# Kernel tuning notes

Measured on AMD Instinct MI355X. Metric: run time of the kernel, lower is better.

The kernel has to match this reference:

```python
import jax, jax.numpy as jnp
import numpy as np

EPS = 1e-5
N_HEADS = 8
CLAMP = 100.0


def layernorm(x, g, b):
    m = x.mean(-1, keepdims=True)
    v = x.var(-1, keepdims=True)  # biased var, matches torch LayerNorm
    return (x - m) / jnp.sqrt(v + EPS) * g + b


def depthwise7(x, w, b):
    # x: [B,C,H,W], w: [C,1,7,7] depthwise (groups=C), pad=3
    y = jax.lax.conv_general_dilated(
        x, w, window_strides=(1, 1), padding=[(3, 3), (3, 3)],
        dimension_numbers=('NCHW', 'OIHW', 'NCHW'),
        feature_group_count=x.shape[1])
    return y + b[None, :, None, None]


def setup_inputs() -> dict:
    key = jax.random.key(0)
    ks = jax.random.split(key, 12)
    B, N, C = 8, 4096, 512
    KH = 7
    s = 0.02
    return {
        'x': jax.random.normal(ks[0], (B, N, C), jnp.float32),
        'qkv_w': jax.random.normal(ks[1], (C, 3 * C), jnp.float32) * s,
        'qkv_b': jnp.zeros((3 * C,), jnp.float32),
        'out_w': jax.random.normal(ks[2], (C, C), jnp.float32) * s,
        'out_b': jnp.zeros((C,), jnp.float32),
        'pre_g': jnp.ones((C,), jnp.float32),
        'pre_b': jnp.zeros((C,), jnp.float32),
        'lcm_g': jnp.ones((C,), jnp.float32),
        'lcm_b': jnp.zeros((C,), jnp.float32),
        'ci_w': jax.random.normal(ks[3], (C, 1, KH, KH), jnp.float32) * s,
        'ci_b': jnp.zeros((C,), jnp.float32),
        'bn_g': jnp.ones((C,), jnp.float32),
        'bn_b': jnp.zeros((C,), jnp.float32),
        'co_w': jax.random.normal(ks[4], (C, 1, KH, KH), jnp.float32) * s,
        'co_b': jnp.zeros((C,), jnp.float32),
        'H': 64,
        'W': 64,
    }


def reference(x, qkv_w, qkv_b, out_w, out_b, pre_g, pre_b, lcm_g, lcm_b,
              ci_w, ci_b, bn_g, bn_b, co_w, co_b, H, W):
    B, N, C = x.shape
    hd = C // N_HEADS
    normed = layernorm(x, pre_g, pre_b)
    qkv = normed @ qkv_w + qkv_b                       # [B,N,3C]
    qkv = qkv.reshape(B, N, 3, N_HEADS, hd).transpose(2, 0, 3, 1, 4)
    q = jax.nn.relu(qkv[0])                            # [B,h,N,d]
    k = jax.nn.relu(qkv[1])
    v = qkv[2]
    kv = jnp.einsum('bhnd,bhnv->bhdv', k, v)           # O(N d^2) associativity trick
    normalizer = jnp.maximum(k.sum(2, keepdims=True), CLAMP)  # [B,h,1,d]
    attn = jnp.einsum('bhnd,bhdv->bhnv', q, kv)
    denom = jnp.maximum((q * normalizer).sum(-1, keepdims=True), CLAMP)
    attn = attn / denom
    attn = attn.transpose(0, 2, 1, 3).reshape(B, N, C)
    attn = attn @ out_w + out_b
    # Local Concentration Module on lcm_norm(attn)
    t = layernorm(attn, lcm_g, lcm_b)
    xi = t.transpose(0, 2, 1).reshape(B, C, H, W)
    y = depthwise7(xi, ci_w, ci_b)
    y = jax.nn.gelu(y, approximate=False)
    m = y.mean((0, 2, 3), keepdims=True)               # BatchNorm2d training-mode stats
    var = y.var((0, 2, 3), keepdims=True)
    y = (y - m) / jnp.sqrt(var + EPS) * bn_g[None, :, None, None] + bn_b[None, :, None, None]
    y = depthwise7(y, co_w, co_b)
    lcm_out = y.reshape(B, C, N).transpose(0, 2, 1)
    return x + attn + lcm_out
```

## Files before the change

kernel.cpp:

```cpp
#include <hip/hip_runtime.h>
#include <math.h>

typedef short v8s __attribute__((ext_vector_type(8)));
typedef short v4s __attribute__((ext_vector_type(4)));
typedef float v4f __attribute__((ext_vector_type(4)));

__device__ __forceinline__ float b2f(unsigned short u) {
    return __uint_as_float(((unsigned)u) << 16);
}
__device__ __forceinline__ unsigned short f2b(float f) {
    unsigned u = __float_as_uint(f);
    unsigned r = (u + 0x7FFF + ((u >> 16) & 1)) >> 16;
    return (unsigned short)r;
}
__device__ __forceinline__ int swz8(int row) { return (row & 7) ^ ((row >> 3) & 7); }

__device__ __forceinline__ void gl_lds16(const unsigned short* g, unsigned short* l) {
    __builtin_amdgcn_global_load_lds(
        (const __attribute__((address_space(1))) void*)g,
        (__attribute__((address_space(3))) void*)l,
        16, 0, 0);
}

__global__ __launch_bounds__(256) void zero_fill(float* __restrict__ p, int n) {
    int i = blockIdx.x * 256 + threadIdx.x;
    if (i < n) p[i] = 0.0f;
}

__global__ __launch_bounds__(256) void ln_apply(const float* __restrict__ x,
                                                const float* __restrict__ g,
                                                const float* __restrict__ bt,
                                                unsigned short* __restrict__ out) {
    size_t row = blockIdx.x;
    const float2* p = (const float2*)(x + row * 512);
    int t = threadIdx.x;
    float2 v = p[t];
    float s = v.x + v.y, s2 = v.x * v.x + v.y * v.y;
    for (int o = 32; o > 0; o >>= 1) {
        s += __shfl_down(s, o);
        s2 += __shfl_down(s2, o);
    }
    __shared__ float rs[4], rq[4];
    int wave = t >> 6, lane = t & 63;
    if (lane == 0) { rs[wave] = s; rq[wave] = s2; }
    __syncthreads();
    float ts = rs[0] + rs[1] + rs[2] + rs[3];
    float tq = rq[0] + rq[1] + rq[2] + rq[3];
    float mean = ts * (1.0f / 512.0f);
    float var = tq * (1.0f / 512.0f) - mean * mean;
    float inv = rsqrtf(var + 1e-5f);
    float2 gg = ((const float2*)g)[t];
    float2 bb = ((const float2*)bt)[t];
    ushort2 o2;
    o2.x = f2b((v.x - mean) * inv * gg.x + bb.x);
    o2.y = f2b((v.y - mean) * inv * gg.y + bb.y);
    *(ushort2*)&out[row * 512 + 2 * t] = o2;
}

__global__ __launch_bounds__(256) void transpose_f2b(const float* __restrict__ in,
                                                     unsigned short* __restrict__ out,
                                                     int R, int C) {
    __shared__ unsigned short tile[32][33];
    int c0 = blockIdx.x * 32, r0 = blockIdx.y * 32;
    int tx = threadIdx.x, ty = threadIdx.y;
    for (int j = 0; j < 32; j += 8)
        tile[ty + j][tx] = f2b(in[(size_t)(r0 + ty + j) * C + c0 + tx]);
    __syncthreads();
    for (int j = 0; j < 32; j += 8)
        out[(size_t)(c0 + ty + j) * R + r0 + tx] = tile[tx][ty + j];
}

template <int NB, bool QKV>
__global__ __launch_bounds__(512, 4) void gemm256(const unsigned short* __restrict__ A,
                                                  const unsigned short* __restrict__ Bt,
                                                  const float* __restrict__ bias,
                                                  unsigned short* __restrict__ o0,
                                                  unsigned short* __restrict__ o1,
                                                  unsigned short* __restrict__ o2) {
    __shared__ __align__(16) unsigned short LB[3][12288];
    int t = threadIdx.x;
    int wave = t >> 6, lane = t & 63;
    int wm = wave >> 1, wn = wave & 1;
    int mrow = lane & 15, kq4 = lane >> 4;
    int nwg = gridDim.x;
    int cpx = nwg >> 3;
    int bid = blockIdx.x;
    int swz = (bid & 7) * cpx + (bid >> 3);
    int n0 = (swz % NB) * 128;
    int m0 = (swz / NB) * 256;
    const unsigned short* Ab = A + (size_t)m0 * 512;
    const unsigned short* Bb = Bt + (size_t)n0 * 512;
    int rA0 = t >> 2;
    int cA0 = (((t & 3) ^ ((rA0 >> 1) & 3)) * 8);
    int rA1 = 128 + (t >> 2);
    int cA1 = (((t & 3) ^ ((rA1 >> 1) & 3)) * 8);
    size_t srcA0 = (size_t)rA0 * 512 + cA0;
    size_t srcA1 = (size_t)rA1 * 512 + cA1;
    unsigned offA0 = wave * 512;
    unsigned offA1 = 4096 + wave * 512;
    unsigned offB  = 8192 + wave * 512;
    v4f acc[4][4] = {};
    int swr = ((kq4 ^ ((mrow >> 1) & 3)) * 8);

#define STAGE(kt, slot)                                          \
    do {                                                         \
        const unsigned short* aS = Ab + (size_t)(kt) * 32;       \
        const unsigned short* bS = Bb + (size_t)(kt) * 32;       \
        gl_lds16(aS + srcA0, &LB[slot][offA0]);                  \
        gl_lds16(aS + srcA1, &LB[slot][offA1]);                  \
        gl_lds16(bS + srcA0, &LB[slot][offB]);                   \
    } while (0)

    STAGE(0, 0);
    STAGE(1, 1);
    for (int kt = 0; kt < 16; ++kt) {
        if (kt < 15) {
            asm volatile("s_waitcnt vmcnt(3)" ::: "memory");
        } else {
            asm volatile("s_waitcnt vmcnt(0)" ::: "memory");
        }
        __builtin_amdgcn_s_barrier();
        asm volatile("" ::: "memory");
        if (kt + 2 < 16) STAGE(kt + 2, (kt + 2) % 3);
        const unsigned short* as = LB[kt % 3];
        const unsigned short* bs = LB[kt % 3] + 8192;
        v8s af[4], bf[4];
#pragma unroll
        for (int i = 0; i < 4; i++)
            af[i] = *(const v8s*)&as[(wm * 64 + i * 16 + mrow) * 32 + swr];
#pragma unroll
        for (int j = 0; j < 4; j++)
            bf[j] = *(const v8s*)&bs[(wn * 64 + j * 16 + mrow) * 32 + swr];
        __builtin_amdgcn_s_setprio(1);
#pragma unroll
        for (int i = 0; i < 4; i++)
#pragma unroll
            for (int j = 0; j < 4; j++)
                acc[i][j] = __builtin_amdgcn_mfma_f32_16x16x32_bf16(af[i], bf[j], acc[i][j], 0, 0, 0);
        __builtin_amdgcn_s_setprio(0);
    }
#undef STAGE
    __syncthreads();
    unsigned short* CT = &LB[0][0];
    bool doRelu = QKV && (n0 < 1024);
#pragma unroll
    for (int j = 0; j < 4; j++) {
        int col = wn * 64 + j * 16 + mrow;
        float bv = bias[n0 + col];
        int gr = col >> 3, gb = col & 7;
#pragma unroll
        for (int i = 0; i < 4; i++) {
            int rowb = wm * 64 + i * 16 + kq4 * 4;
#pragma unroll
            for (int r = 0; r < 4; r++) {
                int row = rowb + r;
                float v = acc[i][j][r] + bv;
                if (doRelu) v = fmaxf(v, 0.0f);
                CT[row * 136 + ((gr ^ swz8(row)) << 3) + gb] = f2b(v);
            }
        }
    }
    __syncthreads();
    if (!QKV || n0 < 512) {
#pragma unroll
        for (int p = 0; p < 8; p++) {
            int g = p * 512 + t;
            int row = g >> 4, gl = g & 15;
            v8s v = *(const v8s*)&CT[row * 136 + ((gl ^ swz8(row)) << 3)];
            *(v8s*)&o0[(size_t)(m0 + row) * 512 + n0 + gl * 8] = v;
        }
    } else {
        unsigned short* Tb = (n0 < 1024) ? o1 : o2;
        int col = t >> 2, sub = t & 3;
        int cglob = n0 + col;
        int hl = (cglob & 511) >> 6, d = cglob & 63;
        int bb = m0 >> 12, gc = m0 & 4095;
        unsigned short* dst = Tb + ((size_t)((bb * 8 + hl) * 64 + d)) * 4096 + gc;
        int cg = col >> 3, cb7 = col & 7;
#pragma unroll
        for (int g = 0; g < 8; g++) {
            v8s v;
#pragma unroll
            for (int e = 0; e < 8; e++) {
                int rr = g * 32 + sub * 8 + e;
                v[e] = (short)CT[rr * 136 + ((cg ^ swz8(rr)) << 3) + cb7];
            }
            *(v8s*)&dst[g * 32 + sub * 8] = v;
        }
    }
}

__global__ __launch_bounds__(256) void kv_part(const unsigned short* __restrict__ kT,
                                               const unsigned short* __restrict__ vT,
                                               float* __restrict__ kvp,
                                               float* __restrict__ ksp) {
    __shared__ __align__(16) unsigned short LB[3][4096];
    int bh = blockIdx.x, nc = blockIdx.y;
    int t = threadIdx.x;
    int w = t >> 6, lane = t & 63;
    int wdk = w >> 1, wdv = w & 1;
    int mrow = lane & 15, kq4 = lane >> 4;
    const unsigned short* Kb = kT + (size_t)bh * 262144 + nc * 512;
    const unsigned short* Vb = vT + (size_t)bh * 262144 + nc * 512;
    int rA = t >> 2;
    int lcA = (t & 3) ^ (rA & 3);
    size_t srcoff = (size_t)rA * 4096 + lcA * 8;
    unsigned dstK = w * 512;
    unsigned dstV = 2048 + w * 512;
    v4f acc[2][2] = {};
    v4f accs[2] = {};
    v8s ones;
#pragma unroll
    for (int jj = 0; jj < 8; jj++) ones[jj] = (short)0x3F80;

#define KSTAGE(ks, slot)                                         \
    do {                                                         \
        gl_lds16(Kb + (size_t)(ks) * 32 + srcoff, &LB[slot][dstK]); \
        gl_lds16(Vb + (size_t)(ks) * 32 + srcoff, &LB[slot][dstV]); \
    } while (0)

    KSTAGE(0, 0);
    KSTAGE(1, 1);
    for (int ks = 0; ks < 16; ++ks) {
        if (ks < 15) {
            asm volatile("s_waitcnt vmcnt(2)" ::: "memory");
        } else {
            asm volatile("s_waitcnt vmcnt(0)" ::: "memory");
        }
        __builtin_amdgcn_s_barrier();
        asm volatile("" ::: "memory");
        if (ks + 2 < 16) KSTAGE(ks + 2, (ks + 2) % 3);
        const unsigned short* as = LB[ks % 3];
        v8s af[2], bf[2];
#pragma unroll
        for (int i = 0; i < 2; i++) {
            int row = wdk * 32 + i * 16 + mrow;
            af[i] = *(const v8s*)&as[row * 32 + ((kq4 ^ (row & 3)) << 3)];
        }
#pragma unroll
        for (int j = 0; j < 2; j++) {
            int row = wdv * 32 + j * 16 + mrow;
            bf[j] = *(const v8s*)&as[2048 + row * 32 + ((kq4 ^ (row & 3)) << 3)];
        }
#pragma unroll
        for (int i = 0; i < 2; i++)
#pragma unroll
            for (int j = 0; j < 2; j++)
                acc[i][j] = __builtin_amdgcn_mfma_f32_16x16x32_bf16(af[i], bf[j], acc[i][j], 0, 0, 0);
        if (wdv == 0) {
#pragma unroll
            for (int i = 0; i < 2; i++)
                accs[i] = __builtin_amdgcn_mfma_f32_16x16x32_bf16(af[i], ones, accs[i], 0, 0, 0);
        }
    }
#undef KSTAGE
    float* dst = kvp + ((size_t)(bh * 8 + nc)) * 4096;
#pragma unroll
    for (int i = 0; i < 2; i++)
#pragma unroll
        for (int j = 0; j < 2; j++)
#pragma unroll
            for (int r = 0; r < 4; r++) {
                int row = wdk * 32 + i * 16 + kq4 * 4 + r;
                int col = wdv * 32 + j * 16 + mrow;
                dst[row * 64 + col] = acc[i][j][r];
            }
    if (wdv == 0 && mrow == 0) {
        float* kd = ksp + ((size_t)(bh * 8 + nc)) * 64 + wdk * 32;
#pragma unroll
        for (int i = 0; i < 2; i++)
#pragma unroll
            for (int r = 0; r < 4; r++)
                kd[i * 16 + kq4 * 4 + r] = accs[i][r];
    }
}

__global__ __launch_bounds__(256) void kv_reduce(const float* __restrict__ kvp,
                                                 const float* __restrict__ ksp,
                                                 float* __restrict__ kvb,
                                                 float* __restrict__ ksum) {
    int tid = blockIdx.x * 256 + threadIdx.x;
    int bh = tid >> 12, e = tid & 4095;
    float s = 0.0f;
#pragma unroll
    for (int c = 0; c < 8; c++) s += kvp[((size_t)(bh * 8 + c)) * 4096 + e];
    kvb[(size_t)bh * 4096 + e] = s;
    if (tid < 4096) {
        int bh2 = tid >> 6, dk = tid & 63;
        float x = 0.0f;
#pragma unroll
        for (int c = 0; c < 8; c++) x += ksp[(bh2 * 8 + c) * 64 + dk];
        ksum[tid] = x;
    }
}

__global__ __launch_bounds__(256) void attn_mfma(unsigned short* __restrict__ qa,
                                                 const float* __restrict__ kv,
                                                 const float* __restrict__ ksum) {
    __shared__ __align__(16) unsigned short olds[4][4096];
    int bh = blockIdx.y;
    int b = bh >> 3, h = bh & 7;
    int t = threadIdx.x;
    int w = t >> 6, lane = t & 63;
    int mrow = lane & 15, kq4 = lane >> 6 ? 0 : lane >> 4;
    kq4 = lane >> 4;
    int nb = blockIdx.x * 256 + w * 64;
    unsigned short* qbase = qa + ((size_t)(b * 4096 + nb)) * 512 + h * 64;
    const float* kvb = kv + (size_t)bh * 4096;
    v4f acc[4][4] = {};
    v4f accd[4] = {};
#pragma unroll
    for (int s = 0; s < 2; s++) {
        v8s af[4];
#pragma unroll
        for (int i = 0; i < 4; i++)
            af[i] = *(const v8s*)&qbase[(size_t)(i * 16 + mrow) * 512 + s * 32 + kq4 * 8];
        v8s nh, nl;
#pragma unroll
        for (int jj = 0; jj < 8; jj++) {
            float nv = fmaxf(ksum[bh * 64 + s * 32 + kq4 * 8 + jj], 100.0f);
            unsigned short hb = f2b(nv);
            nh[jj] = (short)hb;
            nl[jj] = (short)f2b(nv - b2f(hb));
        }
#pragma unroll
        for (int i = 0; i < 4; i++) {
            accd[i] = __builtin_amdgcn_mfma_f32_16x16x32_bf16(af[i], nh, accd[i], 0, 0, 0);
            accd[i] = __builtin_amdgcn_mfma_f32_16x16x32_bf16(af[i], nl, accd[i], 0, 0, 0);
        }
#pragma unroll
        for (int j = 0; j < 4; j++) {
            v8s kh, kl;
#pragma unroll
            for (int jj = 0; jj < 8; jj++) {
                float kvv = kvb[(size_t)(s * 32 + kq4 * 8 + jj) * 64 + j * 16 + mrow];
                unsigned short hb = f2b(kvv);
                kh[jj] = (short)hb;
                kl[jj] = (short)f2b(kvv - b2f(hb));
            }
#pragma unroll
            for (int i = 0; i < 4; i++) {
                acc[i][j] = __builtin_amdgcn_mfma_f32_16x16x32_bf16(af[i], kh, acc[i][j], 0, 0, 0);
                acc[i][j] = __builtin_amdgcn_mfma_f32_16x16x32_bf16(af[i], kl, acc[i][j], 0, 0, 0);
            }
        }
    }
    unsigned short* ol = olds[w];
#pragma unroll
    for (int i = 0; i < 4; i++) {
        float inv[4];
#pragma unroll
        for (int r = 0; r < 4; r++) inv[r] = 1.0f / fmaxf(accd[i][r], 100.0f);
#pragma unroll
        for (int j = 0; j < 4; j++) {
            int dv = j * 16 + mrow;
#pragma unroll
            for (int r = 0; r < 4; r++) {
                int rl = i * 16 + kq4 * 4 + r;
                ol[rl * 64 + (((dv >> 3) ^ (rl & 7)) << 3) + (dv & 7)] = f2b(acc[i][j][r] * inv[r]);
            }
        }
    }
    __syncthreads();
#pragma unroll
    for (int p = 0; p < 8; p++) {
        int idx = p * 64 + lane;
        int row = idx >> 3, gl = idx & 7;
        v8s v = *(const v8s*)&ol[row * 64 + ((gl ^ (row & 7)) << 3)];
        *(v8s*)&qbase[(size_t)row * 512 + gl * 8] = v;
    }
}

__global__ __launch_bounds__(256) void ln2_transpose(const unsigned short* __restrict__ in,
                                                     const float* __restrict__ g,
                                                     const float* __restrict__ bt,
                                                     unsigned short* __restrict__ out) {
    int bid = blockIdx.x;
    int b = bid >> 6;
    int n0 = (bid & 63) * 64;
    __shared__ float gs[512], bs[512];
    __shared__ __align__(16) unsigned short tile[512 * 64];
    int t = threadIdx.x;
    for (int i = t; i < 512; i += 256) { gs[i] = g[i]; bs[i] = bt[i]; }
    int nl = t >> 2, sub = t & 3;
    const unsigned short* src = in + ((size_t)(b * 4096 + n0 + nl)) * 512 + sub * 8;
    v8s vv[16];
#pragma unroll
    for (int c16 = 0; c16 < 16; c16++)
        vv[c16] = *(const v8s*)&src[c16 * 32];
    float s = 0.f, s2 = 0.f;
#pragma unroll
    for (int c16 = 0; c16 < 16; c16++)
#pragma unroll
        for (int j = 0; j < 8; j++) {
            float f = b2f((unsigned short)vv[c16][j]);
            s += f; s2 += f * f;
        }
    s += __shfl_xor(s, 1); s2 += __shfl_xor(s2, 1);
    s += __shfl_xor(s, 2); s2 += __shfl_xor(s2, 2);
    float mean = s * (1.f / 512.f);
    float var = s2 * (1.f / 512.f) - mean * mean;
    float inv = rsqrtf(var + 1e-5f);
    __syncthreads();
#pragma unroll
    for (int c16 = 0; c16 < 16; c16++) {
        int cb_ = sub * 8 + c16 * 32;
#pragma unroll
        for (int j = 0; j < 8; j++) {
            int c = cb_ + j;
            float f = b2f((unsigned short)vv[c16][j]);
            float y = (f - mean) * inv * gs[c] + bs[c];
            tile[c * 64 + ((((nl >> 3) ^ (c & 7)) << 3) | (nl & 7))] = f2b(y);
        }
    }
    __syncthreads();
    unsigned short* dst = out + ((size_t)b * 512) * 4096 + n0;
#pragma unroll
    for (int p = 0; p < 16; p++) {
        int chunk = p * 256 + t;
        int c = chunk >> 3, gseg = chunk & 7;
        int phys = gseg ^ (c & 7);
        v8s v = *(const v8s*)&tile[c * 64 + phys * 8];
        *(v8s*)&dst[(size_t)c * 4096 + gseg * 8] = v;
    }
}

__global__ __launch_bounds__(256) void dwconv7_gelu(const unsigned short* __restrict__ in,
                                                    const float* __restrict__ w,
                                                    const float* __restrict__ bias,
                                                    unsigned short* __restrict__ out,
                                                    float* __restrict__ bn_sum,
                                                    float* __restrict__ bn_sumsq) {
    int bc = blockIdx.x;
    int c = bc & 511;
    __shared__ float img[70 * 72];
    __shared__ float wsm[49];
    __shared__ float r1[4], r2[4];
    int t = threadIdx.x;
    int tx = t & 63, ty = t >> 6;
    for (int i = t; i < 70 * 72; i += 256) img[i] = 0.0f;
    if (t < 49) wsm[t] = w[c * 49 + t];
    __syncthreads();
    const unsigned short* src = in + (size_t)bc * 4096;
#pragma unroll
    for (int q = t; q < 512; q += 256) {
        v8s v = *(const v8s*)&src[q * 8];
        float* ip = &img[((q >> 3) + 3) * 72 + (q & 7) * 8 + 3];
#pragma unroll
        for (int j = 0; j < 8; j++) ip[j] = b2f((unsigned short)v[j]);
    }
    __syncthreads();
    float wt[49];
#pragma unroll
    for (int i = 0; i < 49; i++) wt[i] = wsm[i];
    float bv = bias[c];
    float acc[16];
#pragma unroll
    for (int i = 0; i < 16; i++) acc[i] = bv;
    int h0 = ty * 16;
#pragma unroll
    for (int rr = 0; rr < 22; rr++) {
        float v[7];
#pragma unroll
        for (int kw = 0; kw < 7; kw++) v[kw] = img[(h0 + rr) * 72 + tx + kw];
#pragma unroll
        for (int kh = 0; kh < 7; kh++) {
            int o = rr - kh;
            if (o >= 0 && o <= 15) {
                float dot = v[0] * wt[kh * 7];
#pragma unroll
                for (int kw = 1; kw < 7; kw++) dot += v[kw] * wt[kh * 7 + kw];
                acc[o] += dot;
            }
        }
    }
    float s = 0.0f, s2 = 0.0f;
    unsigned short* dst = out + (size_t)bc * 4096;
#pragma unroll
    for (int i = 0; i < 16; i++) {
        float a = acc[i];
        float ge = 0.5f * a * (1.0f + erff(a * 0.70710678118f));
        dst[(h0 + i) * 64 + tx] = f2b(ge);
        s += ge;
        s2 += ge * ge;
    }
    for (int o = 32; o > 0; o >>= 1) {
        s += __shfl_down(s, o);
        s2 += __shfl_down(s2, o);
    }
    int lane = t & 63;
    if (lane == 0) { r1[ty] = s; r2[ty] = s2; }
    __syncthreads();
    if (t == 0) {
        atomicAdd(&bn_sum[c], r1[0] + r1[1] + r1[2] + r1[3]);
        atomicAdd(&bn_sumsq[c], r2[0] + r2[1] + r2[2] + r2[3]);
    }
}

__global__ void bn_finalize(const float* __restrict__ s, const float* __restrict__ s2,
                            const float* __restrict__ g, const float* __restrict__ b,
                            float2* __restrict__ ab) {
    int c = blockIdx.x * blockDim.x + threadIdx.x;
    if (c >= 512) return;
    float m = s[c] * (1.0f / 32768.0f);
    float var = s2[c] * (1.0f / 32768.0f) - m * m;
    float inv = rsqrtf(var + 1e-5f);
    float sc = g[c] * inv;
    ab[c] = make_float2(sc, b[c] - m * sc);
}

__global__ __launch_bounds__(256) void dwconv7_bn(const unsigned short* __restrict__ in,
                                                  const float2* __restrict__ bnab,
                                                  const float* __restrict__ w,
                                                  const float* __restrict__ bias,
                                                  unsigned short* __restrict__ out) {
    int bc = blockIdx.x;
    int c = bc & 511;
    __shared__ float img[70 * 72];
    __shared__ float wsm[49];
    int t = threadIdx.x;
    int tx = t & 63, ty = t >> 6;
    for (int i = t; i < 70 * 72; i += 256) img[i] = 0.0f;
    if (t < 49) wsm[t] = w[c * 49 + t];
    __syncthreads();
    float2 ab = bnab[c];
    const unsigned short* src = in + (size_t)bc * 4096;
#pragma unroll
    for (int q = t; q < 512; q += 256) {
        v8s v = *(const v8s*)&src[q * 8];
        float* ip = &img[((q >> 3) + 3) * 72 + (q & 7) * 8 + 3];
#pragma unroll
        for (int j = 0; j < 8; j++) ip[j] = b2f((unsigned short)v[j]) * ab.x + ab.y;
    }
    __syncthreads();
    float wt[49];
#pragma unroll
    for (int i = 0; i < 49; i++) wt[i] = wsm[i];
    float bv = bias[c];
    float acc[16];
#pragma unroll
    for (int i = 0; i < 16; i++) acc[i] = bv;
    int h0 = ty * 16;
#pragma unroll
    for (int rr = 0; rr < 22; rr++) {
        float v[7];
#pragma unroll
        for (int kw = 0; kw < 7; kw++) v[kw] = img[(h0 + rr) * 72 + tx + kw];
#pragma unroll
        for (int kh = 0; kh < 7; kh++) {
            int o = rr - kh;
            if (o >= 0 && o <= 15) {
                float dot = v[0] * wt[kh * 7];
#pragma unroll
                for (int kw = 1; kw < 7; kw++) dot += v[kw] * wt[kh * 7 + kw];
                acc[o] += dot;
            }
        }
    }
    unsigned short* dst = out + (size_t)bc * 4096;
#pragma unroll
    for (int i = 0; i < 16; i++)
        dst[(h0 + i) * 64 + tx] = f2b(acc[i]);
}

__global__ __launch_bounds__(256) void final_add(const float* __restrict__ x,
                                                 const unsigned short* __restrict__ attn,
                                                 const unsigned short* __restrict__ y2,
                                                 float* __restrict__ out) {
    __shared__ unsigned short tile[32][36];
    int b = blockIdx.z;
    int c0 = blockIdx.x * 32, n0 = blockIdx.y * 32;
    int t = threadIdx.x;
    {
        int c = t >> 3, n4 = (t & 7) * 4;
        ushort4 v = *(const ushort4*)&y2[((size_t)(b * 512 + c0 + c)) * 4096 + n0 + n4];
        tile[c][n4] = v.x; tile[c][n4 + 1] = v.y; tile[c][n4 + 2] = v.z; tile[c][n4 + 3] = v.w;
    }
    __syncthreads();
    int nl = t >> 3, cl = (t & 7) * 4;
    size_t idx = ((size_t)(b * 4096 + n0 + nl)) * 512 + c0 + cl;
    float4 xv = *(const float4*)&x[idx];
    ushort4 av = *(const ushort4*)&attn[idx];
    float4 o;
    o.x = xv.x + b2f(av.x) + b2f(tile[cl][nl]);
    o.y = xv.y + b2f(av.y) + b2f(tile[cl + 1][nl]);
    o.z = xv.z + b2f(av.z) + b2f(tile[cl + 2][nl]);
    o.w = xv.w + b2f(av.w) + b2f(tile[cl + 3][nl]);
    *(float4*)&out[idx] = o;
}

extern "C" void kernel_launch(void* const* d_in, const int* in_sizes, int n_in,
                              void* d_out, int out_size, void* d_ws, size_t ws_size,
                              hipStream_t stream) {
    const float* x     = (const float*)d_in[0];
    const float* qkv_w = (const float*)d_in[1];
    const float* qkv_b = (const float*)d_in[2];
    const float* out_w = (const float*)d_in[3];
    const float* out_b = (const float*)d_in[4];
    const float* pre_g = (const float*)d_in[5];
    const float* pre_b = (const float*)d_in[6];
    const float* lcm_g = (const float*)d_in[7];
    const float* lcm_b = (const float*)d_in[8];
    const float* ci_w  = (const float*)d_in[9];
    const float* ci_b  = (const float*)d_in[10];
    const float* bn_g  = (const float*)d_in[11];
    const float* bn_b  = (const float*)d_in[12];
    const float* co_w  = (const float*)d_in[13];
    const float* co_b  = (const float*)d_in[14];

    char* ws = (char*)d_ws;
    const size_t SLOT = 33554432;
    unsigned short* S0 = (unsigned short*)(ws);
    unsigned short* S1 = (unsigned short*)(ws + SLOT);
    unsigned short* S2 = (unsigned short*)(ws + 2 * SLOT);
    const size_t MISC = 3 * SLOT;
    unsigned short* wT1 = (unsigned short*)(ws + MISC);
    unsigned short* wT2 = (unsigned short*)(ws + MISC + 1572864);
    float* kvb          = (float*)(ws + MISC + 2097152);
    float* ksum         = (float*)(ws + MISC + 2097152 + 1048576);
    float* bn_sum       = (float*)(ws + MISC + 2097152 + 1048576 + 16384);
    float* bn_sumsq     = (float*)(ws + MISC + 2097152 + 1048576 + 16384 + 2048);
    float2* bnab        = (float2*)(ws + MISC + 3166208);
    float* ksp          = (float*)(ws + MISC + 3170304);
    float* outp         = (float*)d_out;

    unsigned short* normed = (unsigned short*)d_out;
    float* kvp             = (float*)((char*)d_out + SLOT);

    dim3 tb(32, 8);
    transpose_f2b<<<dim3(48, 16), tb, 0, stream>>>(qkv_w, wT1, 512, 1536);
    transpose_f2b<<<dim3(16, 16), tb, 0, stream>>>(out_w, wT2, 512, 512);
    zero_fill<<<4, 256, 0, stream>>>(bn_sum, 1024);
    ln_apply<<<32768, 256, 0, stream>>>(x, pre_g, pre_b, normed);
    gemm256<12, true><<<1536, 512, 0, stream>>>(normed, wT1, qkv_b, S0, S1, S2);
    kv_part<<<dim3(64, 8), 256, 0, stream>>>(S1, S2, kvp, ksp);
    kv_reduce<<<1024, 256, 0, stream>>>(kvp, ksp, kvb, ksum);
    attn_mfma<<<dim3(16, 64), 256, 0, stream>>>(S0, kvb, ksum);
    gemm256<4, false><<<512, 512, 0, stream>>>(S0, wT2, out_b, S1, S1, S1);
    ln2_transpose<<<512, 256, 0, stream>>>(S1, lcm_g, lcm_b, S0);
    dwconv7_gelu<<<4096, 256, 0, stream>>>(S0, ci_w, ci_b, S2, bn_sum, bn_sumsq);
    bn_finalize<<<2, 256, 0, stream>>>(bn_sum, bn_sumsq, bn_g, bn_b, bnab);
    dwconv7_bn<<<4096, 256, 0, stream>>>(S2, bnab, co_w, co_b, S0);
    final_add<<<dim3(16, 128, 8), tb.x * tb.y, 0, stream>>>(x, S1, S0, outp);
}
```

Before: 436.5 us.

## Double-buffer GEMM fragments, one-wave LayerNorm rows, precomputed split-bf16 kv, bigger final_add blocks

The GEMM main loop now preloads the next k-step's LDS fragments into registers between two halves of the MFMAs. This hides LDS read latency behind matrix math, at the cost of more registers. LayerNorm now processes one row per wave with 8 elements per lane, dropping the shared-memory reduction and block barrier. kv_reduce now writes the kv matrix and the clamped normalizer pre-split into high and low bf16 halves in transposed layout, so attn_mfma does vector loads instead of per-element strided loads and conversions. final_add handles four tiles per block to cut the launch block count.

```diff
diff --git a/kernel.cpp b/kernel.cpp
--- a/kernel.cpp
+++ b/kernel.cpp
@@ -31,30 +31,36 @@
                                                 const float* __restrict__ g,
                                                 const float* __restrict__ bt,
                                                 unsigned short* __restrict__ out) {
-    size_t row = blockIdx.x;
-    const float2* p = (const float2*)(x + row * 512);
-    int t = threadIdx.x;
-    float2 v = p[t];
-    float s = v.x + v.y, s2 = v.x * v.x + v.y * v.y;
+    int t = threadIdx.x;
+    int lane = t & 63, wave = t >> 6;
+    size_t row = (size_t)blockIdx.x * 4 + wave;
+    const float* p = x + row * 512 + lane * 8;
+    float4 va = *(const float4*)p;
+    float4 vb = *(const float4*)(p + 4);
+    float s = va.x + va.y + va.z + va.w + vb.x + vb.y + vb.z + vb.w;
+    float s2 = va.x * va.x + va.y * va.y + va.z * va.z + va.w * va.w +
+               vb.x * vb.x + vb.y * vb.y + vb.z * vb.z + vb.w * vb.w;
     for (int o = 32; o > 0; o >>= 1) {
-        s += __shfl_down(s, o);
-        s2 += __shfl_down(s2, o);
-    }
-    __shared__ float rs[4], rq[4];
-    int wave = t >> 6, lane = t & 63;
-    if (lane == 0) { rs[wave] = s; rq[wave] = s2; }
-    __syncthreads();
-    float ts = rs[0] + rs[1] + rs[2] + rs[3];
-    float tq = rq[0] + rq[1] + rq[2] + rq[3];
-    float mean = ts * (1.0f / 512.0f);
-    float var = tq * (1.0f / 512.0f) - mean * mean;
+        s += __shfl_xor(s, o);
+        s2 += __shfl_xor(s2, o);
+    }
+    float mean = s * (1.0f / 512.0f);
+    float var = s2 * (1.0f / 512.0f) - mean * mean;
     float inv = rsqrtf(var + 1e-5f);
-    float2 gg = ((const float2*)g)[t];
-    float2 bb = ((const float2*)bt)[t];
-    ushort2 o2;
-    o2.x = f2b((v.x - mean) * inv * gg.x + bb.x);
-    o2.y = f2b((v.y - mean) * inv * gg.y + bb.y);
-    *(ushort2*)&out[row * 512 + 2 * t] = o2;
+    float4 g0 = *(const float4*)(g + lane * 8);
+    float4 g1 = *(const float4*)(g + lane * 8 + 4);
+    float4 b0 = *(const float4*)(bt + lane * 8);
+    float4 b1 = *(const float4*)(bt + lane * 8 + 4);
+    v8s o8;
+    o8[0] = (short)f2b((va.x - mean) * inv * g0.x + b0.x);
+    o8[1] = (short)f2b((va.y - mean) * inv * g0.y + b0.y);
+    o8[2] = (short)f2b((va.z - mean) * inv * g0.z + b0.z);
+    o8[3] = (short)f2b((va.w - mean) * inv * g0.w + b0.w);
+    o8[4] = (short)f2b((vb.x - mean) * inv * g1.x + b1.x);
+    o8[5] = (short)f2b((vb.y - mean) * inv * g1.y + b1.y);
+    o8[6] = (short)f2b((vb.z - mean) * inv * g1.z + b1.z);
+    o8[7] = (short)f2b((vb.w - mean) * inv * g1.w + b1.w);
+    *(v8s*)&out[row * 512 + lane * 8] = o8;
 }
 
 __global__ __launch_bounds__(256) void transpose_f2b(const float* __restrict__ in,
@@ -113,31 +119,57 @@
 
     STAGE(0, 0);
     STAGE(1, 1);
+    asm volatile("s_waitcnt vmcnt(3)" ::: "memory");
+    __builtin_amdgcn_s_barrier();
+    asm volatile("" ::: "memory");
+    v8s cA[4], cB[4];
+    {
+        const unsigned short* as = LB[0];
+        const unsigned short* bs = as + 8192;
+#pragma unroll
+        for (int i = 0; i < 4; i++) {
+            cA[i] = *(const v8s*)&as[(wm * 64 + i * 16 + mrow) * 32 + swr];
+            cB[i] = *(const v8s*)&bs[(wn * 64 + i * 16 + mrow) * 32 + swr];
+        }
+    }
+#pragma unroll
     for (int kt = 0; kt < 16; ++kt) {
-        if (kt < 15) {
-            asm volatile("s_waitcnt vmcnt(3)" ::: "memory");
-        } else {
-            asm volatile("s_waitcnt vmcnt(0)" ::: "memory");
-        }
         __builtin_amdgcn_s_barrier();
         asm volatile("" ::: "memory");
         if (kt + 2 < 16) STAGE(kt + 2, (kt + 2) % 3);
-        const unsigned short* as = LB[kt % 3];
-        const unsigned short* bs = LB[kt % 3] + 8192;
-        v8s af[4], bf[4];
-#pragma unroll
-        for (int i = 0; i < 4; i++)
-            af[i] = *(const v8s*)&as[(wm * 64 + i * 16 + mrow) * 32 + swr];
-#pragma unroll
-        for (int j = 0; j < 4; j++)
-            bf[j] = *(const v8s*)&bs[(wn * 64 + j * 16 + mrow) * 32 + swr];
         __builtin_amdgcn_s_setprio(1);
 #pragma unroll
-        for (int i = 0; i < 4; i++)
+        for (int i = 0; i < 2; i++)
 #pragma unroll
             for (int j = 0; j < 4; j++)
-                acc[i][j] = __builtin_amdgcn_mfma_f32_16x16x32_bf16(af[i], bf[j], acc[i][j], 0, 0, 0);
+                acc[i][j] = __builtin_amdgcn_mfma_f32_16x16x32_bf16(cA[i], cB[j], acc[i][j], 0, 0, 0);
+        v8s nA[4], nB[4];
+        if (kt < 15) {
+            if (kt < 14) {
+                asm volatile("s_waitcnt vmcnt(3)" ::: "memory");
+            } else {
+                asm volatile("s_waitcnt vmcnt(0)" ::: "memory");
+            }
+            __builtin_amdgcn_s_barrier();
+            asm volatile("" ::: "memory");
+            const unsigned short* as = LB[(kt + 1) % 3];
+            const unsigned short* bs = as + 8192;
+#pragma unroll
+            for (int i = 0; i < 4; i++) {
+                nA[i] = *(const v8s*)&as[(wm * 64 + i * 16 + mrow) * 32 + swr];
+                nB[i] = *(const v8s*)&bs[(wn * 64 + i * 16 + mrow) * 32 + swr];
+            }
+        }
+#pragma unroll
+        for (int i = 2; i < 4; i++)
+#pragma unroll
+            for (int j = 0; j < 4; j++)
+                acc[i][j] = __builtin_amdgcn_mfma_f32_16x16x32_bf16(cA[i], cB[j], acc[i][j], 0, 0, 0);
         __builtin_amdgcn_s_setprio(0);
+        if (kt < 15) {
+#pragma unroll
+            for (int i = 0; i < 4; i++) { cA[i] = nA[i]; cB[i] = nB[i]; }
+        }
     }
 #undef STAGE
     __syncthreads();
@@ -277,36 +309,42 @@
 
 __global__ __launch_bounds__(256) void kv_reduce(const float* __restrict__ kvp,
                                                  const float* __restrict__ ksp,
-                                                 float* __restrict__ kvb,
-                                                 float* __restrict__ ksum) {
+                                                 unsigned short* __restrict__ kvhT,
+                                                 unsigned short* __restrict__ kvlT,
+                                                 unsigned short* __restrict__ nrmp) {
     int tid = blockIdx.x * 256 + threadIdx.x;
     int bh = tid >> 12, e = tid & 4095;
+    int dk = e >> 6, dv = e & 63;
     float s = 0.0f;
 #pragma unroll
     for (int c = 0; c < 8; c++) s += kvp[((size_t)(bh * 8 + c)) * 4096 + e];
-    kvb[(size_t)bh * 4096 + e] = s;
+    unsigned short hb = f2b(s);
+    kvhT[(size_t)bh * 4096 + dv * 64 + dk] = hb;
+    kvlT[(size_t)bh * 4096 + dv * 64 + dk] = f2b(s - b2f(hb));
     if (tid < 4096) {
-        int bh2 = tid >> 6, dk = tid & 63;
+        int bh2 = tid >> 6, dk2 = tid & 63;
         float x = 0.0f;
 #pragma unroll
-        for (int c = 0; c < 8; c++) x += ksp[(bh2 * 8 + c) * 64 + dk];
-        ksum[tid] = x;
+        for (int c = 0; c < 8; c++) x += ksp[(bh2 * 8 + c) * 64 + dk2];
+        x = fmaxf(x, 100.0f);
+        unsigned short nh = f2b(x);
+        nrmp[bh2 * 128 + dk2] = nh;
+        nrmp[bh2 * 128 + 64 + dk2] = f2b(x - b2f(nh));
     }
 }
 
 __global__ __launch_bounds__(256) void attn_mfma(unsigned short* __restrict__ qa,
-                                                 const float* __restrict__ kv,
-                                                 const float* __restrict__ ksum) {
+                                                 const unsigned short* __restrict__ kvhT,
+                                                 const unsigned short* __restrict__ kvlT,
+                                                 const unsigned short* __restrict__ nrmp) {
     __shared__ __align__(16) unsigned short olds[4][4096];
     int bh = blockIdx.y;
     int b = bh >> 3, h = bh & 7;
     int t = threadIdx.x;
     int w = t >> 6, lane = t & 63;
-    int mrow = lane & 15, kq4 = lane >> 6 ? 0 : lane >> 4;
-    kq4 = lane >> 4;
+    int mrow = lane & 15, kq4 = lane >> 4;
     int nb = blockIdx.x * 256 + w * 64;
     unsigned short* qbase = qa + ((size_t)(b * 4096 + nb)) * 512 + h * 64;
-    const float* kvb = kv + (size_t)bh * 4096;
     v4f acc[4][4] = {};
     v4f accd[4] = {};
 #pragma unroll
@@ -315,14 +353,8 @@
 #pragma unroll
         for (int i = 0; i < 4; i++)
             af[i] = *(const v8s*)&qbase[(size_t)(i * 16 + mrow) * 512 + s * 32 + kq4 * 8];
-        v8s nh, nl;
-#pragma unroll
-        for (int jj = 0; jj < 8; jj++) {
-            float nv = fmaxf(ksum[bh * 64 + s * 32 + kq4 * 8 + jj], 100.0f);
-            unsigned short hb = f2b(nv);
-            nh[jj] = (short)hb;
-            nl[jj] = (short)f2b(nv - b2f(hb));
-        }
+        v8s nh = *(const v8s*)&nrmp[bh * 128 + s * 32 + kq4 * 8];
+        v8s nl = *(const v8s*)&nrmp[bh * 128 + 64 + s * 32 + kq4 * 8];
 #pragma unroll
         for (int i = 0; i < 4; i++) {
             accd[i] = __builtin_amdgcn_mfma_f32_16x16x32_bf16(af[i], nh, accd[i], 0, 0, 0);
@@ -330,14 +362,8 @@
         }
 #pragma unroll
         for (int j = 0; j < 4; j++) {
-            v8s kh, kl;
-#pragma unroll
-            for (int jj = 0; jj < 8; jj++) {
-                float kvv = kvb[(size_t)(s * 32 + kq4 * 8 + jj) * 64 + j * 16 + mrow];
-                unsigned short hb = f2b(kvv);
-                kh[jj] = (short)hb;
-                kl[jj] = (short)f2b(kvv - b2f(hb));
-            }
+            v8s kh = *(const v8s*)&kvhT[(size_t)bh * 4096 + (j * 16 + mrow) * 64 + s * 32 + kq4 * 8];
+            v8s kl = *(const v8s*)&kvlT[(size_t)bh * 4096 + (j * 16 + mrow) * 64 + s * 32 + kq4 * 8];
 #pragma unroll
             for (int i = 0; i < 4; i++) {
                 acc[i][j] = __builtin_amdgcn_mfma_f32_16x16x32_bf16(af[i], kh, acc[i][j], 0, 0, 0);
@@ -569,24 +595,30 @@
                                                  float* __restrict__ out) {
     __shared__ unsigned short tile[32][36];
     int b = blockIdx.z;
-    int c0 = blockIdx.x * 32, n0 = blockIdx.y * 32;
-    int t = threadIdx.x;
-    {
-        int c = t >> 3, n4 = (t & 7) * 4;
-        ushort4 v = *(const ushort4*)&y2[((size_t)(b * 512 + c0 + c)) * 4096 + n0 + n4];
-        tile[c][n4] = v.x; tile[c][n4 + 1] = v.y; tile[c][n4 + 2] = v.z; tile[c][n4 + 3] = v.w;
-    }
-    __syncthreads();
-    int nl = t >> 3, cl = (t & 7) * 4;
-    size_t idx = ((size_t)(b * 4096 + n0 + nl)) * 512 + c0 + cl;
-    float4 xv = *(const float4*)&x[idx];
-    ushort4 av = *(const ushort4*)&attn[idx];
-    float4 o;
-    o.x = xv.x + b2f(av.x) + b2f(tile[cl][nl]);
-    o.y = xv.y + b2f(av.y) + b2f(tile[cl + 1][nl]);
-    o.z = xv.z + b2f(av.z) + b2f(tile[cl + 2][nl]);
-    o.w = xv.w + b2f(av.w) + b2f(tile[cl + 3][nl]);
-    *(float4*)&out[idx] = o;
+    int c0 = blockIdx.x * 32;
+    int n0b = blockIdx.y * 128;
+    int t = threadIdx.x;
+#pragma unroll
+    for (int nt = 0; nt < 4; ++nt) {
+        int n0 = n0b + nt * 32;
+        __syncthreads();
+        {
+            int c = t >> 3, n4 = (t & 7) * 4;
+            ushort4 v = *(const ushort4*)&y2[((size_t)(b * 512 + c0 + c)) * 4096 + n0 + n4];
+            tile[c][n4] = v.x; tile[c][n4 + 1] = v.y; tile[c][n4 + 2] = v.z; tile[c][n4 + 3] = v.w;
+        }
+        __syncthreads();
+        int nl = t >> 3, cl = (t & 7) * 4;
+        size_t idx = ((size_t)(b * 4096 + n0 + nl)) * 512 + c0 + cl;
+        float4 xv = *(const float4*)&x[idx];
+        ushort4 av = *(const ushort4*)&attn[idx];
+        float4 o;
+        o.x = xv.x + b2f(av.x) + b2f(tile[cl][nl]);
+        o.y = xv.y + b2f(av.y) + b2f(tile[cl + 1][nl]);
+        o.z = xv.z + b2f(av.z) + b2f(tile[cl + 2][nl]);
+        o.w = xv.w + b2f(av.w) + b2f(tile[cl + 3][nl]);
+        *(float4*)&out[idx] = o;
+    }
 }
 
 extern "C" void kernel_launch(void* const* d_in, const int* in_sizes, int n_in,
@@ -616,30 +648,31 @@
     const size_t MISC = 3 * SLOT;
     unsigned short* wT1 = (unsigned short*)(ws + MISC);
     unsigned short* wT2 = (unsigned short*)(ws + MISC + 1572864);
-    float* kvb          = (float*)(ws + MISC + 2097152);
-    float* ksum         = (float*)(ws + MISC + 2097152 + 1048576);
-    float* bn_sum       = (float*)(ws + MISC + 2097152 + 1048576 + 16384);
-    float* bn_sumsq     = (float*)(ws + MISC + 2097152 + 1048576 + 16384 + 2048);
-    float2* bnab        = (float2*)(ws + MISC + 3166208);
-    float* ksp          = (float*)(ws + MISC + 3170304);
+    float* bn_sum       = (float*)(ws + MISC + 2097152);
+    float* bn_sumsq     = (float*)(ws + MISC + 2097152 + 2048);
+    float2* bnab        = (float2*)(ws + MISC + 2097152 + 4096);
+    float* ksp          = (float*)(ws + MISC + 2105344);
     float* outp         = (float*)d_out;
 
     unsigned short* normed = (unsigned short*)d_out;
     float* kvp             = (float*)((char*)d_out + SLOT);
+    unsigned short* kvhT   = (unsigned short*)((char*)d_out + SLOT + 8388608);
+    unsigned short* kvlT   = kvhT + 262144;
+    unsigned short* nrmp   = kvlT + 262144;
 
     dim3 tb(32, 8);
     transpose_f2b<<<dim3(48, 16), tb, 0, stream>>>(qkv_w, wT1, 512, 1536);
     transpose_f2b<<<dim3(16, 16), tb, 0, stream>>>(out_w, wT2, 512, 512);
     zero_fill<<<4, 256, 0, stream>>>(bn_sum, 1024);
-    ln_apply<<<32768, 256, 0, stream>>>(x, pre_g, pre_b, normed);
+    ln_apply<<<8192, 256, 0, stream>>>(x, pre_g, pre_b, normed);
     gemm256<12, true><<<1536, 512, 0, stream>>>(normed, wT1, qkv_b, S0, S1, S2);
     kv_part<<<dim3(64, 8), 256, 0, stream>>>(S1, S2, kvp, ksp);
-    kv_reduce<<<1024, 256, 0, stream>>>(kvp, ksp, kvb, ksum);
-    attn_mfma<<<dim3(16, 64), 256, 0, stream>>>(S0, kvb, ksum);
+    kv_reduce<<<1024, 256, 0, stream>>>(kvp, ksp, kvhT, kvlT, nrmp);
+    attn_mfma<<<dim3(16, 64), 256, 0, stream>>>(S0, kvhT, kvlT, nrmp);
     gemm256<4, false><<<512, 512, 0, stream>>>(S0, wT2, out_b, S1, S1, S1);
     ln2_transpose<<<512, 256, 0, stream>>>(S1, lcm_g, lcm_b, S0);
     dwconv7_gelu<<<4096, 256, 0, stream>>>(S0, ci_w, ci_b, S2, bn_sum, bn_sumsq);
     bn_finalize<<<2, 256, 0, stream>>>(bn_sum, bn_sumsq, bn_g, bn_b, bnab);
     dwconv7_bn<<<4096, 256, 0, stream>>>(S2, bnab, co_w, co_b, S0);
-    final_add<<<dim3(16, 128, 8), tb.x * tb.y, 0, stream>>>(x, S1, S0, outp);
-}
+    final_add<<<dim3(16, 32, 8), 256, 0, stream>>>(x, S1, S0, outp);
+}
```

Result: faster. 419.9 us (-3.8%).
